# Optimization experiments

Measured on AMD Instinct MI355X. Metric: run time of the kernel, lower is better.

## Reference

```python
import jax, jax.numpy as jnp
import numpy as np

D_MODEL = 768
N_HEADS = 12
HEAD_DIM = D_MODEL // N_HEADS
BIAS_HIDDEN = 32


def setup_inputs() -> dict:
    key = jax.random.key(0)
    ks = jax.random.split(key, 16)
    B, L = 4, 1024
    std = 0.02
    inp = {
        "x": jax.random.normal(ks[0], (B, L, D_MODEL), dtype=jnp.float32),
        "spatial_pos": jax.random.uniform(ks[1], (B, L, 2), dtype=jnp.float32),
        "Wq": jax.random.normal(ks[2], (D_MODEL, D_MODEL), dtype=jnp.float32) * std,
        "bq": jnp.zeros((D_MODEL,), dtype=jnp.float32),
        "Wk": jax.random.normal(ks[3], (D_MODEL, D_MODEL), dtype=jnp.float32) * std,
        "bk": jnp.zeros((D_MODEL,), dtype=jnp.float32),
        "Wv": jax.random.normal(ks[4], (D_MODEL, D_MODEL), dtype=jnp.float32) * std,
        "bv": jnp.zeros((D_MODEL,), dtype=jnp.float32),
        "Wo": jax.random.normal(ks[5], (D_MODEL, D_MODEL), dtype=jnp.float32) * std,
        "bo": jnp.zeros((D_MODEL,), dtype=jnp.float32),
        "W1": jax.random.normal(ks[6], (2, BIAS_HIDDEN), dtype=jnp.float32) * 0.5,
        "b1": jnp.zeros((BIAS_HIDDEN,), dtype=jnp.float32),
        "W2": jax.random.normal(ks[7], (BIAS_HIDDEN, N_HEADS), dtype=jnp.float32) * 0.5,
        "b2": jnp.zeros((N_HEADS,), dtype=jnp.float32),
    }
    return inp


def reference(x, spatial_pos, Wq, bq, Wk, bk, Wv, bv, Wo, bo, W1, b1, W2, b2):
    B, L, D = x.shape
    H, hd = N_HEADS, HEAD_DIM
    scale = hd ** (-0.5)

    q = (x @ Wq + bq).reshape(B, L, H, hd)  # [B,L,H,hd]
    k = (x @ Wk + bk).reshape(B, L, H, hd)
    v = (x @ Wv + bv).reshape(B, L, H, hd)

    # scores: [B,H,L,L]
    attn = jnp.einsum("bihd,bjhd->bhij", q, k) * scale

    # pairwise spatial deltas: [B,L,L,2]
    delta = spatial_pos[:, :, None, :] - spatial_pos[:, None, :, :]
    hidden = jax.nn.relu(delta @ W1 + b1)          # [B,L,L,32]
    bias = hidden @ W2 + b2                        # [B,L,L,H]
    attn = attn + jnp.transpose(bias, (0, 3, 1, 2))

    attn = jax.nn.softmax(attn, axis=-1)
    out = jnp.einsum("bhij,bjhd->bihd", attn, v).reshape(B, L, D)
    return out @ Wo + bo
```

## Files before the change

### kernel.cpp

```cpp
#include <hip/hip_runtime.h>
#include <hip/hip_fp16.h>


typedef unsigned short ushort_t;
typedef unsigned int uint_t;
typedef __attribute__((ext_vector_type(8))) short bf16x8;
typedef __attribute__((ext_vector_type(4))) float f32x4;

__device__ __forceinline__ ushort_t f2b(float f) {
    union { float f; uint_t u; } v;
    v.f = f;
    uint_t r = v.u + 0x7fffu + ((v.u >> 16) & 1u);
    return (ushort_t)(r >> 16);
}
__device__ __forceinline__ float b2f(ushort_t b) {
    union { uint_t u; float f; } v;
    v.u = ((uint_t)b) << 16;
    return v.f;
}

__device__ __forceinline__ void gload16(const void* g, void* l) {
    __builtin_amdgcn_global_load_lds(
        (const __attribute__((address_space(1))) unsigned int*)g,
        (__attribute__((address_space(3))) unsigned int*)l, 16, 0, 0);
}

__global__ __launch_bounds__(256) void split_hi_lo(const float* __restrict__ X,
                                                   ushort_t* __restrict__ X2) {
    const int idx = blockIdx.x * 256 + threadIdx.x;
    const int m = idx / 192, k4 = (idx - m * 192) * 4;
    float4 v = *(const float4*)&X[(size_t)m * 768 + k4];
    ushort4 hi, lo;
    hi.x = f2b(v.x); lo.x = f2b(v.x - b2f(hi.x));
    hi.y = f2b(v.y); lo.y = f2b(v.y - b2f(hi.y));
    hi.z = f2b(v.z); lo.z = f2b(v.z - b2f(hi.z));
    hi.w = f2b(v.w); lo.w = f2b(v.w - b2f(hi.w));
    ushort_t* row = X2 + (size_t)m * 1536;
    *(ushort4*)&row[k4]       = hi;
    *(ushort4*)&row[768 + k4] = lo;
}

__global__ __launch_bounds__(256) void split_wT(const float* __restrict__ W,
                                                ushort_t* __restrict__ Wt,
                                                int n_base) {
    __shared__ float Ws[64][65];
    const int t = threadIdx.x;
    const int rr0 = blockIdx.x * 64, nn0 = blockIdx.y * 64;
    const int c = t & 63, r4 = t >> 6;
#pragma unroll
    for (int e = 0; e < 16; ++e) {
        const int r = r4 + e * 4;
        Ws[r][c] = W[(size_t)(rr0 + r) * 768 + nn0 + c];
    }
    __syncthreads();
#pragma unroll
    for (int e = 0; e < 16; ++e) {
        const int nloc = r4 + e * 4;
        const float v = Ws[c][nloc];
        const ushort_t h = f2b(v);
        const ushort_t l = f2b(v - b2f(h));
        ushort_t* rowp = Wt + (size_t)(n_base + nn0 + nloc) * 1536 + rr0 + c;
        rowp[0]   = h;
        rowp[768] = l;
    }
}

__device__ __forceinline__ void kmap(int s, int& ka, int& kb) {
    const int phase = s / 12;
    const int q = s - phase * 12;
    ka = ((phase == 2) ? 768 : 0) + q * 64;
    kb = ((phase == 1) ? 768 : 0) + q * 64;
}

template <int QKV>
__global__ __launch_bounds__(256) void mfma_gemm(
    const ushort_t* __restrict__ A2, const ushort_t* __restrict__ Bt,
    const float* __restrict__ bv0, const float* __restrict__ bv1,
    const float* __restrict__ bv2, ushort_t* __restrict__ Qh,
    ushort_t* __restrict__ Ql, ushort_t* __restrict__ Kh,
    ushort_t* __restrict__ Kl, ushort_t* __restrict__ Vth,
    ushort_t* __restrict__ Vtl, float* __restrict__ C0) {
    __shared__ ushort_t As[2][128 * 64];
    __shared__ ushort_t Bs[2][128 * 64];

    const int t = threadIdx.x;
    const int w = t >> 6, lane = t & 63;

    const int nbx = QKV ? 18 : 6;
    const int lid0 = blockIdx.y * nbx + blockIdx.x;
    const int cpx = (nbx * 32) >> 3;
    const int lid = (lid0 & 7) * cpx + (lid0 >> 3);
    const int n0 = (lid % nbx) * 128;
    const int m0 = (lid / nbx) * 128;

    const int wr = (w >> 1) * 64, wc = (w & 1) * 64;

    f32x4 acc[4][4];
#pragma unroll
    for (int i = 0; i < 4; ++i)
#pragma unroll
        for (int j = 0; j < 4; ++j) acc[i][j] = (f32x4){0.f, 0.f, 0.f, 0.f};

    const int srow = t >> 3;
    const int sslot = t & 7;

    auto STAGE = [&](int buf, int ka, int kb) {
#pragma unroll
        for (int it = 0; it < 4; ++it) {
            const int row = srow + it * 32;
            const int sw8 = ((sslot ^ (row & 7)) << 3);
            char* dstA = (char*)&As[buf][0] + it * 4096 + w * 1024;
            char* dstB = (char*)&Bs[buf][0] + it * 4096 + w * 1024;
            gload16(A2 + (size_t)(m0 + row) * 1536 + ka + sw8, dstA);
            gload16(Bt + (size_t)(n0 + row) * 1536 + kb + sw8, dstB);
        }
    };

    auto COMPUTE = [&](int buf) {
#pragma unroll
        for (int kk = 0; kk < 2; ++kk) {
            bf16x8 a[4], b[4];
#pragma unroll
            for (int i = 0; i < 4; ++i) {
                const int ra = wr + i * 16 + (lane & 15);
                const int sa = ((kk << 2) + (lane >> 4)) ^ (ra & 7);
                a[i] = *(const bf16x8*)((const char*)&As[buf][0] + ra * 128 + sa * 16);
                const int rb = wc + i * 16 + (lane & 15);
                const int sb = ((kk << 2) + (lane >> 4)) ^ (rb & 7);
                b[i] = *(const bf16x8*)((const char*)&Bs[buf][0] + rb * 128 + sb * 16);
            }
#pragma unroll
            for (int i = 0; i < 4; ++i)
#pragma unroll
                for (int j = 0; j < 4; ++j)
                    acc[i][j] = __builtin_amdgcn_mfma_f32_16x16x32_bf16(
                        a[i], b[j], acc[i][j], 0, 0, 0);
        }
    };

    int ka, kb;
    kmap(0, ka, kb);
    STAGE(0, ka, kb);
    __syncthreads();
    int cur = 0;
    for (int s = 0; s < 35; ++s) {
        kmap(s + 1, ka, kb);
        STAGE(cur ^ 1, ka, kb);
        COMPUTE(cur);
        __syncthreads();
        cur ^= 1;
    }
    COMPUTE(cur);

    const int cl = lane & 15, rg = (lane >> 4) * 4;
    if constexpr (QKV) {
        const int which = n0 / 768;
        const int nb = n0 - which * 768 + wc;
        const float* bb = which == 0 ? bv0 : (which == 1 ? bv1 : bv2);
#pragma unroll
        for (int i = 0; i < 4; ++i)
#pragma unroll
            for (int j = 0; j < 4; ++j) {
                const int cw = nb + j * 16 + cl;
                const int h = cw >> 6, d = cw & 63;
                const float badd = bb[cw];
#pragma unroll
                for (int r = 0; r < 4; ++r) {
                    const int gr = m0 + wr + i * 16 + rg + r;
                    const int b = gr >> 10, l = gr & 1023;
                    const int bh = b * 12 + h;
                    float val = acc[i][j][r] + badd;
                    if (which == 0) val *= 0.125f;
                    const ushort_t hi = f2b(val);
                    const ushort_t lo = f2b(val - b2f(hi));
                    if (which == 0) {
                        const size_t idx = ((size_t)((bh << 10) + l)) * 64 + d;
                        Qh[idx] = hi; Ql[idx] = lo;
                    } else if (which == 1) {
                        const size_t idx = ((size_t)((bh << 10) + l)) * 64 + d;
                        Kh[idx] = hi; Kl[idx] = lo;
                    } else {
                        const size_t idx = (((size_t)((bh << 6) + d)) << 10) + l;
                        Vth[idx] = hi; Vtl[idx] = lo;
                    }
                }
            }
    } else {
#pragma unroll
        for (int i = 0; i < 4; ++i)
#pragma unroll
            for (int j = 0; j < 4; ++j) {
                const int gc = n0 + wc + j * 16 + cl;
#pragma unroll
                for (int r = 0; r < 4; ++r) {
                    const int gr = m0 + wr + i * 16 + rg + r;
                    C0[(size_t)gr * 768 + gc] = acc[i][j][r] + bv0[gc];
                }
            }
    }
}

__global__ __launch_bounds__(256) void bias_mlp(const float* __restrict__ pos,
                                                const float* __restrict__ W1,
                                                const float* __restrict__ b1,
                                                const float* __restrict__ W2,
                                                const float* __restrict__ b2,
                                                __half* __restrict__ Bias) {
    __shared__ float w1x[32], w1y[32], b1s[32], b2s[12];
    __shared__ float w2T[12][32];

    const int t = threadIdx.x;
    const int i = blockIdx.x;
    const int b = blockIdx.y;

    if (t < 32) { w1x[t] = W1[t]; w1y[t] = W1[32 + t]; b1s[t] = b1[t]; }
    if (t >= 32 && t < 44) b2s[t - 32] = b2[t - 32];
    for (int v = t; v < 384; v += 256) {
        const int u = v / 12, hh = v - u * 12;
        w2T[hh][u] = W2[v];
    }
    __syncthreads();

    const float2 pi2 = *(const float2*)&pos[((b << 10) + i) << 1];
    const float4 pj01 = *(const float4*)&pos[((b << 10) + 2 * t) << 1];
    const float4 pj23 = *(const float4*)&pos[((b << 10) + 2 * t + 512) << 1];
    float dx[4], dy[4];
    dx[0] = pi2.x - pj01.x; dy[0] = pi2.y - pj01.y;
    dx[1] = pi2.x - pj01.z; dy[1] = pi2.y - pj01.w;
    dx[2] = pi2.x - pj23.x; dy[2] = pi2.y - pj23.y;
    dx[3] = pi2.x - pj23.z; dy[3] = pi2.y - pj23.w;

    float acc[4][12];
#pragma unroll
    for (int e = 0; e < 4; ++e)
#pragma unroll
        for (int h = 0; h < 12; ++h) acc[e][h] = b2s[h];

#pragma unroll
    for (int u4 = 0; u4 < 8; ++u4) {
        const float4 ax = *(const float4*)&w1x[u4 << 2];
        const float4 ay = *(const float4*)&w1y[u4 << 2];
        const float4 ab = *(const float4*)&b1s[u4 << 2];
        float4 hv[4];
#pragma unroll
        for (int e = 0; e < 4; ++e) {
            hv[e].x = fmaxf(fmaf(dx[e], ax.x, fmaf(dy[e], ay.x, ab.x)), 0.f);
            hv[e].y = fmaxf(fmaf(dx[e], ax.y, fmaf(dy[e], ay.y, ab.y)), 0.f);
            hv[e].z = fmaxf(fmaf(dx[e], ax.z, fmaf(dy[e], ay.z, ab.z)), 0.f);
            hv[e].w = fmaxf(fmaf(dx[e], ax.w, fmaf(dy[e], ay.w, ab.w)), 0.f);
        }
#pragma unroll
        for (int h = 0; h < 12; ++h) {
            const float4 wv = *(const float4*)&w2T[h][u4 << 2];
#pragma unroll
            for (int e = 0; e < 4; ++e)
                acc[e][h] = fmaf(hv[e].x, wv.x,
                            fmaf(hv[e].y, wv.y,
                            fmaf(hv[e].z, wv.z,
                            fmaf(hv[e].w, wv.w, acc[e][h]))));
        }
    }

    const size_t base = (((size_t)(b * 12)) << 20) + (((size_t)i) << 10);
#pragma unroll
    for (int h = 0; h < 12; ++h) {
        const size_t off = base + (((size_t)h) << 20);
        *(__half2*)&Bias[off + 2 * t]       = __floats2half2_rn(acc[0][h], acc[1][h]);
        *(__half2*)&Bias[off + 2 * t + 512] = __floats2half2_rn(acc[2][h], acc[3][h]);
    }
}

__global__ __launch_bounds__(256) void attn_mfma(
    const ushort_t* __restrict__ Qh, const ushort_t* __restrict__ Ql,
    const ushort_t* __restrict__ Kh, const ushort_t* __restrict__ Kl,
    const ushort_t* __restrict__ Vth, const ushort_t* __restrict__ Vtl,
    const __half* __restrict__ BiasT, ushort_t* __restrict__ A2) {
    __shared__ ushort_t Kls[2][64][64];
    __shared__ ushort_t Vls[2][64][64];
    __shared__ ushort_t P2s[4][2][16][64];

    const int t = threadIdx.x;
    const int wgid0 = blockIdx.x;
    const int wgid = (wgid0 & 7) * 96 + (wgid0 >> 3);
    const int bh = wgid >> 4, it = wgid & 15;
    const int b = bh / 12, h = bh - b * 12;
    const int i0 = it << 6;
    const int w = t >> 6, l = t & 63;
    const int l4 = l >> 4, lm = l & 15;

    const __half* bp = BiasT + (((size_t)bh) << 20) +
                       (((size_t)(i0 + 16 * w + l4 * 4)) << 10) + lm;

    const size_t qoff = ((size_t)((bh << 10) + i0 + 16 * w + lm)) * 64 + l4 * 8;
    const bf16x8 qh0 = *(const bf16x8*)(Qh + qoff);
    const bf16x8 qh1 = *(const bf16x8*)(Qh + qoff + 32);
    const bf16x8 ql0 = *(const bf16x8*)(Ql + qoff);
    const bf16x8 ql1 = *(const bf16x8*)(Ql + qoff + 32);

    float m_[4], l_[4];
    f32x4 o_[4];
#pragma unroll
    for (int r = 0; r < 4; ++r) { m_[r] = -1e30f; l_[r] = 0.f; }
#pragma unroll
    for (int db = 0; db < 4; ++db) o_[db] = (f32x4){0.f, 0.f, 0.f, 0.f};

    for (int jt = 0; jt < 16; ++jt) {
        const int j0 = jt << 6;

        float bias_r[4][4];
#pragma unroll
        for (int cb = 0; cb < 4; ++cb)
#pragma unroll
            for (int r = 0; r < 4; ++r)
                bias_r[cb][r] = __half2float(bp[(r << 10) + j0 + 16 * cb]);

        __syncthreads();
        {
            ushort_t* lb = (w == 0) ? &Kls[0][0][0]
                         : (w == 1) ? &Kls[1][0][0]
                         : (w == 2) ? &Vls[0][0][0] : &Vls[1][0][0];
            const ushort_t* gt = (w == 0) ? Kh : (w == 1) ? Kl
                               : (w == 2) ? Vth : Vtl;
#pragma unroll
            for (int ch = 0; ch < 8; ++ch) {
                const int row = ch * 8 + (l >> 3);
                const int off8 = (((l & 7) ^ (row & 7)) << 3);
                const ushort_t* src =
                    (w < 2) ? gt + ((size_t)((bh << 10) + j0 + row)) * 64 + off8
                            : gt + ((size_t)((bh << 6) + row)) * 1024 + j0 + off8;
                gload16(src, (char*)lb + ch * 1024);
            }
        }
        __syncthreads();

        f32x4 s_[4];
#pragma unroll
        for (int cb = 0; cb < 4; ++cb) {
            const int row = 16 * cb + lm;
            const int sw = row & 7;
            const char* k0p = (const char*)&Kls[0][0][0] + row * 128;
            const char* k1p = (const char*)&Kls[1][0][0] + row * 128;
            const bf16x8 kh0 = *(const bf16x8*)(k0p + ((l4 + 0) ^ sw) * 16);
            const bf16x8 kh1 = *(const bf16x8*)(k0p + ((l4 + 4) ^ sw) * 16);
            const bf16x8 kl0 = *(const bf16x8*)(k1p + ((l4 + 0) ^ sw) * 16);
            const bf16x8 kl1 = *(const bf16x8*)(k1p + ((l4 + 4) ^ sw) * 16);
            f32x4 a = (f32x4){0.f, 0.f, 0.f, 0.f};
            a = __builtin_amdgcn_mfma_f32_16x16x32_bf16(qh0, kh0, a, 0, 0, 0);
            a = __builtin_amdgcn_mfma_f32_16x16x32_bf16(qh1, kh1, a, 0, 0, 0);
            a = __builtin_amdgcn_mfma_f32_16x16x32_bf16(qh0, kl0, a, 0, 0, 0);
            a = __builtin_amdgcn_mfma_f32_16x16x32_bf16(qh1, kl1, a, 0, 0, 0);
            a = __builtin_amdgcn_mfma_f32_16x16x32_bf16(ql0, kh0, a, 0, 0, 0);
            a = __builtin_amdgcn_mfma_f32_16x16x32_bf16(ql1, kh1, a, 0, 0, 0);
            s_[cb] = a;
        }

#pragma unroll
        for (int cb = 0; cb < 4; ++cb)
#pragma unroll
            for (int r = 0; r < 4; ++r) s_[cb][r] += bias_r[cb][r];

        float corr[4];
#pragma unroll
        for (int r = 0; r < 4; ++r) {
            float mx = fmaxf(fmaxf(s_[0][r], s_[1][r]), fmaxf(s_[2][r], s_[3][r]));
            mx = fmaxf(mx, __shfl_xor(mx, 1));
            mx = fmaxf(mx, __shfl_xor(mx, 2));
            mx = fmaxf(mx, __shfl_xor(mx, 4));
            mx = fmaxf(mx, __shfl_xor(mx, 8));
            const float mn = fmaxf(m_[r], mx);
            corr[r] = __expf(m_[r] - mn);
            m_[r] = mn;
            float ps = 0.f;
#pragma unroll
            for (int cb = 0; cb < 4; ++cb) {
                s_[cb][r] = __expf(s_[cb][r] - mn);
                ps += s_[cb][r];
            }
            ps += __shfl_xor(ps, 1);
            ps += __shfl_xor(ps, 2);
            ps += __shfl_xor(ps, 4);
            ps += __shfl_xor(ps, 8);
            l_[r] = fmaf(l_[r], corr[r], ps);
            o_[0][r] *= corr[r]; o_[1][r] *= corr[r];
            o_[2][r] *= corr[r]; o_[3][r] *= corr[r];
        }

        char* pw = (char*)&P2s[w][0][0][0];
#pragma unroll
        for (int cb = 0; cb < 4; ++cb)
#pragma unroll
            for (int r = 0; r < 4; ++r) {
                const float p = s_[cb][r];
                const ushort_t ph = f2b(p);
                const ushort_t pl = f2b(p - b2f(ph));
                const int rl = l4 * 4 + r;
                const int bo = rl * 128 + ((((lm >> 3) + 2 * cb) ^ (rl & 7)) << 4)
                               + ((2 * lm) & 15);
                *(ushort_t*)(pw + bo) = ph;
                *(ushort_t*)(pw + 2048 + bo) = pl;
            }

        const int psw = lm & 7;
        const char* pb = (const char*)&P2s[w][0][0][0] + lm * 128;
        const bf16x8 pa0 = *(const bf16x8*)(pb + ((l4 + 0) ^ psw) * 16);
        const bf16x8 pa1 = *(const bf16x8*)(pb + ((l4 + 4) ^ psw) * 16);
        const bf16x8 pb0 = *(const bf16x8*)(pb + 2048 + ((l4 + 0) ^ psw) * 16);
        const bf16x8 pb1 = *(const bf16x8*)(pb + 2048 + ((l4 + 4) ^ psw) * 16);

#pragma unroll
        for (int db = 0; db < 4; ++db) {
            const int vrow = 16 * db + lm;
            const int vw = vrow & 7;
            const char* v0p = (const char*)&Vls[0][0][0] + vrow * 128;
            const char* v1p = (const char*)&Vls[1][0][0] + vrow * 128;
            const bf16x8 vh0 = *(const bf16x8*)(v0p + ((l4 + 0) ^ vw) * 16);
            const bf16x8 vh1 = *(const bf16x8*)(v0p + ((l4 + 4) ^ vw) * 16);
            const bf16x8 vl0 = *(const bf16x8*)(v1p + ((l4 + 0) ^ vw) * 16);
            const bf16x8 vl1 = *(const bf16x8*)(v1p + ((l4 + 4) ^ vw) * 16);
            f32x4 a = o_[db];
            a = __builtin_amdgcn_mfma_f32_16x16x32_bf16(pa0, vh0, a, 0, 0, 0);
            a = __builtin_amdgcn_mfma_f32_16x16x32_bf16(pa1, vh1, a, 0, 0, 0);
            a = __builtin_amdgcn_mfma_f32_16x16x32_bf16(pa0, vl0, a, 0, 0, 0);
            a = __builtin_amdgcn_mfma_f32_16x16x32_bf16(pa1, vl1, a, 0, 0, 0);
            a = __builtin_amdgcn_mfma_f32_16x16x32_bf16(pb0, vh0, a, 0, 0, 0);
            a = __builtin_amdgcn_mfma_f32_16x16x32_bf16(pb1, vh1, a, 0, 0, 0);
            o_[db] = a;
        }
    }

    const int mrow = (b << 10) + i0 + 16 * w + l4 * 4;
#pragma unroll
    for (int r = 0; r < 4; ++r) {
        const float inv = 1.f / l_[r];
        ushort_t* rowp = A2 + (size_t)(mrow + r) * 1536;
#pragma unroll
        for (int db = 0; db < 4; ++db) {
            const float val = o_[db][r] * inv;
            const ushort_t hi = f2b(val);
            const ushort_t lo = f2b(val - b2f(hi));
            const int c = (h << 6) + 16 * db + lm;
            rowp[c] = hi;
            rowp[768 + c] = lo;
        }
    }
}

extern "C" void kernel_launch(void* const* d_in, const int* in_sizes, int n_in,
                              void* d_out, int out_size, void* d_ws, size_t ws_size,
                              hipStream_t stream) {
    const float* x   = (const float*)d_in[0];
    const float* pos = (const float*)d_in[1];
    const float* Wq  = (const float*)d_in[2];
    const float* bq  = (const float*)d_in[3];
    const float* Wk  = (const float*)d_in[4];
    const float* bk  = (const float*)d_in[5];
    const float* Wv  = (const float*)d_in[6];
    const float* bv  = (const float*)d_in[7];
    const float* Wo  = (const float*)d_in[8];
    const float* bo  = (const float*)d_in[9];
    const float* W1  = (const float*)d_in[10];
    const float* b1  = (const float*)d_in[11];
    const float* W2  = (const float*)d_in[12];
    const float* b2  = (const float*)d_in[13];
    float* out = (float*)d_out;

    ushort_t* Qhb = (ushort_t*)d_ws;
    ushort_t* Qlb = Qhb + 3145728;
    ushort_t* Khb = Qlb + 3145728;
    ushort_t* Klb = Khb + 3145728;
    ushort_t* Vth = Klb + 3145728;
    ushort_t* Vtl = Vth + 3145728;
    ushort_t* A2  = Vtl + 3145728;
    ushort_t* W2b = A2 + 6291456;
    __half* BiasH = (__half*)(W2b + 3538944);

    split_hi_lo<<<3072, 256, 0, stream>>>(x, A2);
    split_wT<<<dim3(12, 12), 256, 0, stream>>>(Wq, W2b, 0);
    split_wT<<<dim3(12, 12), 256, 0, stream>>>(Wk, W2b, 768);
    split_wT<<<dim3(12, 12), 256, 0, stream>>>(Wv, W2b, 1536);

    mfma_gemm<1><<<dim3(18, 32), 256, 0, stream>>>(
        A2, W2b, bq, bk, bv, Qhb, Qlb, Khb, Klb, Vth, Vtl, nullptr);

    bias_mlp<<<dim3(1024, 4), 256, 0, stream>>>(pos, W1, b1, W2, b2, BiasH);

    attn_mfma<<<768, 256, 0, stream>>>(Qhb, Qlb, Khb, Klb, Vth, Vtl, BiasH, A2);

    split_wT<<<dim3(12, 12), 256, 0, stream>>>(Wo, W2b, 0);
    mfma_gemm<0><<<dim3(6, 32), 256, 0, stream>>>(
        A2, W2b, bo, nullptr, nullptr, nullptr, nullptr, nullptr, nullptr, nullptr,
        nullptr, out);
}
```

Measured before the change: 393.8 us.

## Restructure split-bf16 GEMM to load hi/lo tiles together; split bias MLP grid

The GEMM main loop now loads the hi and lo halves of A and B for the same 32-wide k slice into four LDS buffers at once. It reuses each A and B fragment for all three hi*hi, hi*lo and lo*hi MFMA products, replacing the earlier 36-step phase sequence that reloaded tiles for each product. The loop is single-buffered with two barriers per step, so global-to-LDS loads no longer overlap with MFMA work. The bias MLP kernel also gains a third grid dimension that halves the work per thread, giving more blocks and lower register pressure.

```diff
diff --git a/kernel.cpp b/kernel.cpp
--- a/kernel.cpp
+++ b/kernel.cpp
@@ -65,13 +65,6 @@
     }
 }
 
-__device__ __forceinline__ void kmap(int s, int& ka, int& kb) {
-    const int phase = s / 12;
-    const int q = s - phase * 12;
-    ka = ((phase == 2) ? 768 : 0) + q * 64;
-    kb = ((phase == 1) ? 768 : 0) + q * 64;
-}
-
 template <int QKV>
 __global__ __launch_bounds__(256) void mfma_gemm(
     const ushort_t* __restrict__ A2, const ushort_t* __restrict__ Bt,
@@ -80,11 +73,11 @@
     ushort_t* __restrict__ Ql, ushort_t* __restrict__ Kh,
     ushort_t* __restrict__ Kl, ushort_t* __restrict__ Vth,
     ushort_t* __restrict__ Vtl, float* __restrict__ C0) {
-    __shared__ ushort_t As[2][128 * 64];
-    __shared__ ushort_t Bs[2][128 * 64];
+    __shared__ ushort_t Ls[4][128 * 32];
 
     const int t = threadIdx.x;
     const int w = t >> 6, lane = t & 63;
+    const int lm = lane & 15, l4 = lane >> 4;
 
     const int nbx = QKV ? 18 : 6;
     const int lid0 = blockIdx.y * nbx + blockIdx.x;
@@ -101,56 +94,62 @@
 #pragma unroll
         for (int j = 0; j < 4; ++j) acc[i][j] = (f32x4){0.f, 0.f, 0.f, 0.f};
 
-    const int srow = t >> 3;
-    const int sslot = t & 7;
-
-    auto STAGE = [&](int buf, int ka, int kb) {
-#pragma unroll
-        for (int it = 0; it < 4; ++it) {
-            const int row = srow + it * 32;
-            const int sw8 = ((sslot ^ (row & 7)) << 3);
-            char* dstA = (char*)&As[buf][0] + it * 4096 + w * 1024;
-            char* dstB = (char*)&Bs[buf][0] + it * 4096 + w * 1024;
-            gload16(A2 + (size_t)(m0 + row) * 1536 + ka + sw8, dstA);
-            gload16(Bt + (size_t)(n0 + row) * 1536 + kb + sw8, dstB);
-        }
-    };
-
-    auto COMPUTE = [&](int buf) {
-#pragma unroll
-        for (int kk = 0; kk < 2; ++kk) {
-            bf16x8 a[4], b[4];
+    const int sr0 = t >> 2, ss0 = t & 3;
+    const int sr1 = (t + 256) >> 2, ss1 = (t + 256) & 3;
+    const int k80 = (ss0 ^ ((sr0 >> 1) & 3)) << 3;
+    const int k81 = (ss1 ^ ((sr1 >> 1) & 3)) << 3;
+
+    const ushort_t* baseA = A2 + (size_t)m0 * 1536;
+    const ushort_t* baseB = Bt + (size_t)n0 * 1536;
+
+    for (int q = 0; q < 24; ++q) {
+        const int k0 = q * 32;
+        __syncthreads();
+        {
+            gload16(baseA + (size_t)sr0 * 1536 + k0 + k80,
+                    (char*)&Ls[0][0] + t * 16);
+            gload16(baseA + (size_t)sr1 * 1536 + k0 + k81,
+                    (char*)&Ls[0][0] + (t + 256) * 16);
+            gload16(baseA + (size_t)sr0 * 1536 + 768 + k0 + k80,
+                    (char*)&Ls[1][0] + t * 16);
+            gload16(baseA + (size_t)sr1 * 1536 + 768 + k0 + k81,
+                    (char*)&Ls[1][0] + (t + 256) * 16);
+            gload16(baseB + (size_t)sr0 * 1536 + k0 + k80,
+                    (char*)&Ls[2][0] + t * 16);
+            gload16(baseB + (size_t)sr1 * 1536 + k0 + k81,
+                    (char*)&Ls[2][0] + (t + 256) * 16);
+            gload16(baseB + (size_t)sr0 * 1536 + 768 + k0 + k80,
+                    (char*)&Ls[3][0] + t * 16);
+            gload16(baseB + (size_t)sr1 * 1536 + 768 + k0 + k81,
+                    (char*)&Ls[3][0] + (t + 256) * 16);
+        }
+        __syncthreads();
+
+        bf16x8 ah[4], al[4];
+#pragma unroll
+        for (int i = 0; i < 4; ++i) {
+            const int ra = wr + i * 16 + lm;
+            const int sa = (l4 ^ ((ra >> 1) & 3)) << 4;
+            ah[i] = *(const bf16x8*)((const char*)&Ls[0][0] + ra * 64 + sa);
+            al[i] = *(const bf16x8*)((const char*)&Ls[1][0] + ra * 64 + sa);
+        }
+#pragma unroll
+        for (int j = 0; j < 4; ++j) {
+            const int rb = wc + j * 16 + lm;
+            const int sb = (l4 ^ ((rb >> 1) & 3)) << 4;
+            const bf16x8 bh = *(const bf16x8*)((const char*)&Ls[2][0] + rb * 64 + sb);
+            const bf16x8 bl = *(const bf16x8*)((const char*)&Ls[3][0] + rb * 64 + sb);
 #pragma unroll
             for (int i = 0; i < 4; ++i) {
-                const int ra = wr + i * 16 + (lane & 15);
-                const int sa = ((kk << 2) + (lane >> 4)) ^ (ra & 7);
-                a[i] = *(const bf16x8*)((const char*)&As[buf][0] + ra * 128 + sa * 16);
-                const int rb = wc + i * 16 + (lane & 15);
-                const int sb = ((kk << 2) + (lane >> 4)) ^ (rb & 7);
-                b[i] = *(const bf16x8*)((const char*)&Bs[buf][0] + rb * 128 + sb * 16);
-            }
-#pragma unroll
-            for (int i = 0; i < 4; ++i)
-#pragma unroll
-                for (int j = 0; j < 4; ++j)
-                    acc[i][j] = __builtin_amdgcn_mfma_f32_16x16x32_bf16(
-                        a[i], b[j], acc[i][j], 0, 0, 0);
-        }
-    };
-
-    int ka, kb;
-    kmap(0, ka, kb);
-    STAGE(0, ka, kb);
-    __syncthreads();
-    int cur = 0;
-    for (int s = 0; s < 35; ++s) {
-        kmap(s + 1, ka, kb);
-        STAGE(cur ^ 1, ka, kb);
-        COMPUTE(cur);
-        __syncthreads();
-        cur ^= 1;
-    }
-    COMPUTE(cur);
+                acc[i][j] = __builtin_amdgcn_mfma_f32_16x16x32_bf16(ah[i], bh,
+                                                                    acc[i][j], 0, 0, 0);
+                acc[i][j] = __builtin_amdgcn_mfma_f32_16x16x32_bf16(ah[i], bl,
+                                                                    acc[i][j], 0, 0, 0);
+                acc[i][j] = __builtin_amdgcn_mfma_f32_16x16x32_bf16(al[i], bh,
+                                                                    acc[i][j], 0, 0, 0);
+            }
+        }
+    }
 
     const int cl = lane & 15, rg = (lane >> 4) * 4;
     if constexpr (QKV) {
@@ -168,19 +167,19 @@
                 for (int r = 0; r < 4; ++r) {
                     const int gr = m0 + wr + i * 16 + rg + r;
                     const int b = gr >> 10, l = gr & 1023;
-                    const int bh = b * 12 + h;
+                    const int bh2 = b * 12 + h;
                     float val = acc[i][j][r] + badd;
                     if (which == 0) val *= 0.125f;
                     const ushort_t hi = f2b(val);
                     const ushort_t lo = f2b(val - b2f(hi));
                     if (which == 0) {
-                        const size_t idx = ((size_t)((bh << 10) + l)) * 64 + d;
+                        const size_t idx = ((size_t)((bh2 << 10) + l)) * 64 + d;
                         Qh[idx] = hi; Ql[idx] = lo;
                     } else if (which == 1) {
-                        const size_t idx = ((size_t)((bh << 10) + l)) * 64 + d;
+                        const size_t idx = ((size_t)((bh2 << 10) + l)) * 64 + d;
                         Kh[idx] = hi; Kl[idx] = lo;
                     } else {
-                        const size_t idx = (((size_t)((bh << 6) + d)) << 10) + l;
+                        const size_t idx = (((size_t)((bh2 << 6) + d)) << 10) + l;
                         Vth[idx] = hi; Vtl[idx] = lo;
                     }
                 }
@@ -212,6 +211,7 @@
     const int t = threadIdx.x;
     const int i = blockIdx.x;
     const int b = blockIdx.y;
+    const int j0 = blockIdx.z * 512;
 
     if (t < 32) { w1x[t] = W1[t]; w1y[t] = W1[32 + t]; b1s[t] = b1[t]; }
     if (t >= 32 && t < 44) b2s[t - 32] = b2[t - 32];
@@ -222,17 +222,14 @@
     __syncthreads();
 
     const float2 pi2 = *(const float2*)&pos[((b << 10) + i) << 1];
-    const float4 pj01 = *(const float4*)&pos[((b << 10) + 2 * t) << 1];
-    const float4 pj23 = *(const float4*)&pos[((b << 10) + 2 * t + 512) << 1];
-    float dx[4], dy[4];
+    const float4 pj01 = *(const float4*)&pos[((b << 10) + j0 + 2 * t) << 1];
+    float dx[2], dy[2];
     dx[0] = pi2.x - pj01.x; dy[0] = pi2.y - pj01.y;
     dx[1] = pi2.x - pj01.z; dy[1] = pi2.y - pj01.w;
-    dx[2] = pi2.x - pj23.x; dy[2] = pi2.y - pj23.y;
-    dx[3] = pi2.x - pj23.z; dy[3] = pi2.y - pj23.w;
-
-    float acc[4][12];
-#pragma unroll
-    for (int e = 0; e < 4; ++e)
+
+    float acc[2][12];
+#pragma unroll
+    for (int e = 0; e < 2; ++e)
 #pragma unroll
         for (int h = 0; h < 12; ++h) acc[e][h] = b2s[h];
 
@@ -241,9 +238,9 @@
         const float4 ax = *(const float4*)&w1x[u4 << 2];
         const float4 ay = *(const float4*)&w1y[u4 << 2];
         const float4 ab = *(const float4*)&b1s[u4 << 2];
-        float4 hv[4];
-#pragma unroll
-        for (int e = 0; e < 4; ++e) {
+        float4 hv[2];
+#pragma unroll
+        for (int e = 0; e < 2; ++e) {
             hv[e].x = fmaxf(fmaf(dx[e], ax.x, fmaf(dy[e], ay.x, ab.x)), 0.f);
             hv[e].y = fmaxf(fmaf(dx[e], ax.y, fmaf(dy[e], ay.y, ab.y)), 0.f);
             hv[e].z = fmaxf(fmaf(dx[e], ax.z, fmaf(dy[e], ay.z, ab.z)), 0.f);
@@ -253,7 +250,7 @@
         for (int h = 0; h < 12; ++h) {
             const float4 wv = *(const float4*)&w2T[h][u4 << 2];
 #pragma unroll
-            for (int e = 0; e < 4; ++e)
+            for (int e = 0; e < 2; ++e)
                 acc[e][h] = fmaf(hv[e].x, wv.x,
                             fmaf(hv[e].y, wv.y,
                             fmaf(hv[e].z, wv.z,
@@ -261,13 +258,11 @@
         }
     }
 
-    const size_t base = (((size_t)(b * 12)) << 20) + (((size_t)i) << 10);
-#pragma unroll
-    for (int h = 0; h < 12; ++h) {
-        const size_t off = base + (((size_t)h) << 20);
-        *(__half2*)&Bias[off + 2 * t]       = __floats2half2_rn(acc[0][h], acc[1][h]);
-        *(__half2*)&Bias[off + 2 * t + 512] = __floats2half2_rn(acc[2][h], acc[3][h]);
-    }
+    const size_t base = (((size_t)(b * 12)) << 20) + (((size_t)i) << 10) + j0;
+#pragma unroll
+    for (int h = 0; h < 12; ++h)
+        *(__half2*)&Bias[base + (((size_t)h) << 20) + 2 * t] =
+            __floats2half2_rn(acc[0][h], acc[1][h]);
 }
 
 __global__ __launch_bounds__(256) void attn_mfma(
@@ -482,7 +477,7 @@
     mfma_gemm<1><<<dim3(18, 32), 256, 0, stream>>>(
         A2, W2b, bq, bk, bv, Qhb, Qlb, Khb, Klb, Vth, Vtl, nullptr);
 
-    bias_mlp<<<dim3(1024, 4), 256, 0, stream>>>(pos, W1, b1, W2, b2, BiasH);
+    bias_mlp<<<dim3(1024, 4, 2), 256, 0, stream>>>(pos, W1, b1, W2, b2, BiasH);
 
     attn_mfma<<<768, 256, 0, stream>>>(Qhb, Qlb, Khb, Klb, Vth, Vtl, BiasH, A2);
 
```

Measured after the change: 335.0 us. 1.18x faster.
